# Kernel optimization log

Measured on AMD Instinct MI355X. Metric: run time of the kernel, lower is better.

Reference implementation:

```python
import jax, jax.numpy as jnp
import numpy as np
from functools import partial

IN_DIM = 128
NUM_HEADS = 8
DOWN_DIM = IN_DIM // 2          # 64
HEAD_DIM = DOWN_DIM // NUM_HEADS  # 8
MID = max(1, DOWN_DIM // 16)    # 4 (gate_reduce=16)
DIL = 3
BN_EPS = 1e-5


def conv2d(x, w, padding=0, dilation=1):
    # x: [B,C,H,W], w: [O,I,kh,kw]
    return jax.lax.conv_general_dilated(
        x, w, window_strides=(1, 1),
        padding=[(padding, padding), (padding, padding)],
        rhs_dilation=(dilation, dilation),
        dimension_numbers=("NCHW", "OIHW", "NCHW"))


def batchnorm(x, gamma, beta, mean, var):
    # inference-mode BN over channel dim
    scale = (gamma / jnp.sqrt(var + BN_EPS))[None, :, None, None]
    shift = (beta - mean * gamma / jnp.sqrt(var + BN_EPS))[None, :, None, None]
    return x * scale + shift


def complex_l2_norm(z, eps=1e-6):
    denom = jnp.sqrt(jnp.sum(z.real ** 2 + z.imag ** 2, axis=-1, keepdims=True) + eps)
    return z / denom


def complex_softmax(z):
    return jax.lax.complex(jax.nn.softmax(z.real, axis=-1),
                           jax.nn.softmax(z.imag, axis=-1))


def setup_inputs() -> dict:
    key = jax.random.key(0)
    ks = jax.random.split(key, 6)
    B, H, W = 8, 128, 128
    inp = {}
    inp["x"] = jax.random.normal(ks[0], (B, IN_DIM, H, W), dtype=jnp.float32)
    inp["conv_w"] = jax.random.normal(ks[1], (DOWN_DIM, IN_DIM, 3, 3), dtype=jnp.float32) * 0.02
    inp["bn1_g"] = jnp.ones((DOWN_DIM,), jnp.float32)
    inp["bn1_b"] = jnp.zeros((DOWN_DIM,), jnp.float32)
    inp["bn1_m"] = jnp.zeros((DOWN_DIM,), jnp.float32)
    inp["bn1_v"] = jnp.ones((DOWN_DIM,), jnp.float32)
    inp["cg1_w"] = jax.random.normal(ks[2], (MID, DOWN_DIM, 1, 1), dtype=jnp.float32) * 0.1
    inp["cg1_b"] = jnp.zeros((MID,), jnp.float32)
    inp["cgbn_g"] = jnp.ones((MID,), jnp.float32)
    inp["cgbn_b"] = jnp.zeros((MID,), jnp.float32)
    inp["cgbn_m"] = jnp.zeros((MID,), jnp.float32)
    inp["cgbn_v"] = jnp.ones((MID,), jnp.float32)
    inp["cg2_w"] = jax.random.normal(ks[3], (DOWN_DIM, MID, 1, 1), dtype=jnp.float32) * 0.1
    inp["cg2_b"] = jnp.zeros((DOWN_DIM,), jnp.float32)
    inp["tau"] = jnp.ones((NUM_HEADS, 1, 1), jnp.float32) * (HEAD_DIM ** -0.5)
    return inp


def reference(x, conv_w, bn1_g, bn1_b, bn1_m, bn1_v,
              cg1_w, cg1_b, cgbn_g, cgbn_b, cgbn_m, cgbn_v,
              cg2_w, cg2_b, tau):
    B, C, H, W = x.shape
    # reduce branch: dilated 3x3 conv -> BN -> GELU (exact, matching torch nn.GELU)
    feat = conv2d(x, conv_w, padding=DIL, dilation=DIL)
    feat = batchnorm(feat, bn1_g, bn1_b, bn1_m, bn1_v)
    feat = jax.nn.gelu(feat, approximate=False)

    # q=k=v=g = fft2(feat) (torch computes four identical FFTs; same math)
    F2 = jnp.fft.fft2(feat.astype(jnp.float32), axes=(-2, -1))  # complex64 [B,64,H,W]
    N = H * W
    qkv = F2.reshape(B, NUM_HEADS, HEAD_DIM, N)  # b h d (H W)
    q = complex_l2_norm(qkv)
    k = complex_l2_norm(qkv)
    v = qkv
    # attn: [b,h,d,d] — tiny; contraction over N
    attn = jnp.einsum("bhdn,bhen->bhde", q, jnp.conj(k)) * tau
    attn = complex_softmax(attn)
    out_f = jnp.einsum("bhde,bhen->bhdn", attn, v)
    out_f = out_f.reshape(B, DOWN_DIM, H, W)
    out_f = jnp.abs(jnp.fft.ifft2(out_f, axes=(-2, -1)))

    # gated branch on g = F2
    gr = F2.real
    cg = conv2d(gr, cg1_w) + cg1_b[None, :, None, None]
    cg = batchnorm(cg, cgbn_g, cgbn_b, cgbn_m, cgbn_v)
    cg = jax.nn.gelu(cg, approximate=False)
    cg = conv2d(cg, cg2_w) + cg2_b[None, :, None, None]
    cg = jax.nn.sigmoid(cg)
    gate = cg * F2  # real gate times complex spectrum
    gate = jnp.abs(jnp.fft.ifft2(gate, axes=(-2, -1)))

    y = jnp.concatenate([out_f, gate], axis=1)
    return y + x
```

## Files before the change

kernel.cpp:

```cpp
#include <hip/hip_runtime.h>
#include <hip/hip_bf16.h>
#include <math.h>

#define NB 8
#define CIN 128
#define CDN 64
#define NPIX 16384
#define NHEADS 8
#define HDIM 8

typedef __attribute__((ext_vector_type(8))) short bf16x8;
typedef __attribute__((ext_vector_type(4))) float f32x4;
typedef __attribute__((ext_vector_type(8))) unsigned short u16x8;

struct alignas(8) c2 { float x, y; };

__device__ inline c2 cadd(c2 a, c2 b){ return {a.x+b.x, a.y+b.y}; }
__device__ inline c2 csub(c2 a, c2 b){ return {a.x-b.x, a.y-b.y}; }
__device__ inline c2 cmul(c2 a, c2 b){ return {a.x*b.x - a.y*b.y, a.x*b.y + a.y*b.x}; }
__device__ inline c2 shfl2(c2 v, int m){ return { __shfl_xor(v.x, m, 64), __shfl_xor(v.y, m, 64) }; }
__device__ inline float gelu_exact(float v){ return 0.5f*v*(1.f + erff(v*0.70710678118654752f)); }
__device__ inline unsigned short f2bf(float f){
  __hip_bfloat16 h = __float2bfloat16(f);
  return *reinterpret_cast<unsigned short*>(&h);
}
__device__ inline float bf2f(unsigned short u){ return __uint_as_float((unsigned)u << 16); }

struct Tw { c2 t0; c2 t[6]; };
__device__ inline void tw_init(Tw& w, int t){
  float sn, cs;
  sincosf(-6.283185307179586f * (float)t * (1.f/128.f), &sn, &cs); w.t0 = {cs, sn};
  #pragma unroll
  for (int i = 0; i < 6; ++i) {
    int sp = 32 >> i;
    int j = t & (sp-1);
    sincosf(-3.141592653589793f * (float)j / (float)sp, &sn, &cs);
    w.t[i] = {cs, sn};
  }
}
__device__ inline void fft128_fwd(c2& a, c2& b, int t, const Tw& w){
  c2 s = cadd(a,b), d = csub(a,b);
  a = s; b = cmul(d, w.t0);
  #pragma unroll
  for (int i = 0; i < 6; ++i) {
    int sp = 32 >> i;
    c2 oa = shfl2(a, sp), ob = shfl2(b, sp);
    c2 tw = w.t[i];
    if (t & sp) { a = cmul(csub(oa,a), tw); b = cmul(csub(ob,b), tw); }
    else        { a = cadd(a,oa);           b = cadd(b,ob); }
  }
}
__device__ inline void fft128_inv(c2& a, c2& b, int t, const Tw& w){
  #pragma unroll
  for (int i = 5; i >= 0; --i) {
    int sp = 32 >> i;
    c2 tw = {w.t[i].x, -w.t[i].y};
    c2 oa = shfl2(a, sp), ob = shfl2(b, sp);
    if (t & sp) { a = csub(oa, cmul(a, tw)); b = csub(ob, cmul(b, tw)); }
    else        { a = cadd(a, cmul(oa, tw)); b = cadd(b, cmul(ob, tw)); }
  }
  c2 t0c = {w.t0.x, -w.t0.y};
  c2 wb = cmul(b, t0c);
  b = csub(a, wb);
  a = cadd(a, wb);
}

__device__ inline void gload_lds16(const void* g, void* l){
  __builtin_amdgcn_global_load_lds(
      (const __attribute__((address_space(1))) unsigned int*)g,
      (__attribute__((address_space(3))) unsigned int*)l, 16, 0, 0);
}

__device__ inline int colmap8(int wv, int i){
  if (wv == 0) return i;
  if (wv == 1) return 8 + i;
  if (wv == 2) return i < 4 ? 16 + i : 24 + i;
  if (wv == 3) return 20 + i;
  if (wv < 8) { int a = wv - 4; return i < 4 ? 32 + 4*a + i : 56 - 4*a + i; }
  int a = wv - 8; return i < 4 ? 64 + 4*a + i : 120 - 4*a + i;
}

__global__ __launch_bounds__(256) void k_wpack(const float* __restrict__ w, unsigned short* __restrict__ wP){
  int idx = blockIdx.x*256 + threadIdx.x;
  if (idx >= 4*9*64*32) return;
  int cc  = idx / 18432;
  int r   = idx - cc*18432;
  int tap = r / 2048;
  int r2  = r - tap*2048;
  int co  = r2 >> 5;
  int cil = r2 & 31;
  int ci  = cc*32 + cil;
  wP[idx] = f2bf(w[(co*CIN + ci)*9 + tap]);
}

__global__ __launch_bounds__(256) void k_xpose(const float* __restrict__ x, unsigned short* __restrict__ xT){
  int b = blockIdx.x >> 6;
  int px = (blockIdx.x & 63)*256 + threadIdx.x;
  const float* xb = x + (size_t)b*CIN*NPIX + px;
  #pragma unroll 2
  for (int ci0 = 0; ci0 < 128; ci0 += 8) {
    u16x8 v;
    #pragma unroll
    for (int j = 0; j < 8; ++j) v[j] = f2bf(xb[(size_t)(ci0+j)*NPIX]);
    int cc = ci0 >> 5;
    *(u16x8*)(xT + (((size_t)(b*4+cc)*NPIX + px)*32 + (ci0 & 31))) = v;
  }
}

__global__ __launch_bounds__(256) void k_conv(const unsigned short* __restrict__ xT,
    const unsigned short* __restrict__ wP,
    const float* __restrict__ bg, const float* __restrict__ bbeta,
    const float* __restrict__ bm, const float* __restrict__ bv,
    const float* __restrict__ w1,
    unsigned short* __restrict__ feat, float* __restrict__ u){
  __shared__ __align__(16) unsigned short sX[512*32];
  __shared__ float w1s[256];
  const int tid = threadIdx.x;
  const int bb   = blockIdx.z;
  const int half = blockIdx.x & 1;
  const int coBase = half*32;
  const int x0 = (blockIdx.x >> 1) * 16, y0 = blockIdx.y * 16;
  const int wv  = tid >> 6;
  const int l   = tid & 63;
  const int l15 = l & 15;
  const int g   = l >> 4;

  w1s[tid] = w1[tid];

  const bool interior = (x0 >= 16) && (x0 <= 96) && (y0 >= 16) && (y0 <= 96);

  f32x4 acc[2][4];
  #pragma unroll
  for (int m=0;m<2;++m)
    #pragma unroll
    for (int n=0;n<4;++n) acc[m][n] = {0.f,0.f,0.f,0.f};

  const int ko = g*8;

  for (int cc = 0; cc < 4; ++cc) {
    __syncthreads();
    const unsigned short* xcc = xT + ((size_t)(bb*4 + cc))*NPIX*32;
    if (interior) {
      #pragma unroll
      for (int k = 0; k < 8; ++k) {
        int blk = k*4 + wv;
        int idx = blk*64 + l;
        int p = idx >> 2, i = idx & 3;
        int pc = p < 484 ? p : 483;
        int py = pc / 22, px = pc - py*22;
        int gpix = (y0-3+py)*128 + (x0-3+px);
        int sg = i ^ ((p >> 1) & 3);
        const unsigned short* srcp = xcc + (size_t)gpix*32 + sg*8;
        gload_lds16(srcp, (char*)sX + blk*1024);
      }
    } else {
      #pragma unroll
      for (int k = 0; k < 8; ++k) {
        int idx = k*256 + tid;
        int p = idx >> 2, i = idx & 3;
        u16x8 v = {0,0,0,0,0,0,0,0};
        if (p < 484) {
          int py = p / 22, px = p - py*22;
          int gy = y0-3+py, gx = x0-3+px;
          if ((unsigned)gy < 128u && (unsigned)gx < 128u) {
            int sg = i ^ ((p >> 1) & 3);
            v = *(const u16x8*)(xcc + (size_t)(gy*128+gx)*32 + sg*8);
          }
        }
        *(u16x8*)((char*)sX + idx*16) = v;
      }
    }
    __syncthreads();

    const unsigned short* wcc = wP + cc*18432;
    for (int tap = 0; tap < 9; ++tap) {
      int dy = (tap/3)*3, dx = (tap - (tap/3)*3)*3;
      const unsigned short* wt = wcc + tap*2048;
      bf16x8 a[2], b[4];
      #pragma unroll
      for (int m = 0; m < 2; ++m)
        a[m] = *reinterpret_cast<const bf16x8*>(wt + (coBase + m*16 + l15)*32 + ko);
      #pragma unroll
      for (int n = 0; n < 4; ++n) {
        int p = (wv*4 + n + dy)*22 + l15 + dx;
        b[n] = *reinterpret_cast<const bf16x8*>(&sX[p*32 + ((g ^ ((p >> 1) & 3)) << 3)]);
      }
      #pragma unroll
      for (int m = 0; m < 2; ++m)
        #pragma unroll
        for (int n = 0; n < 4; ++n)
          acc[m][n] = __builtin_amdgcn_mfma_f32_16x16x32_bf16(a[m], b[n], acc[m][n], 0, 0, 0);
    }
  }

  float up[4][4];
  #pragma unroll
  for (int n=0;n<4;++n)
    #pragma unroll
    for (int m2=0;m2<4;++m2) up[n][m2] = 0.f;

  #pragma unroll
  for (int m = 0; m < 2; ++m) {
    #pragma unroll
    for (int r = 0; r < 4; ++r) {
      int co = coBase + m*16 + g*4 + r;
      float sc = bg[co] * rsqrtf(bv[co] + 1e-5f);
      float sh = bbeta[co] - bm[co]*sc;
      float wv4[4];
      #pragma unroll
      for (int m2 = 0; m2 < 4; ++m2) wv4[m2] = w1s[m2*64 + co];
      #pragma unroll
      for (int n = 0; n < 4; ++n) {
        int py = wv*4 + n;
        float v = gelu_exact(acc[m][n][r]*sc + sh);
        feat[((size_t)(bb*CDN + co)*128 + (y0+py))*128 + x0 + l15] = f2bf(v);
        #pragma unroll
        for (int m2 = 0; m2 < 4; ++m2) up[n][m2] += wv4[m2]*v;
      }
    }
  }
  #pragma unroll
  for (int n=0;n<4;++n)
    #pragma unroll
    for (int m2=0;m2<4;++m2) {
      up[n][m2] += __shfl_xor(up[n][m2], 16, 64);
      up[n][m2] += __shfl_xor(up[n][m2], 32, 64);
    }
  if (g == 0) {
    #pragma unroll
    for (int n = 0; n < 4; ++n) {
      int py = y0 + wv*4 + n;
      #pragma unroll
      for (int m2 = 0; m2 < 4; ++m2)
        u[((size_t)((bb*2 + half)*4 + m2))*NPIX + py*128 + x0 + l15] = up[n][m2];
    }
  }
}

__global__ __launch_bounds__(256) void k_attn1(const unsigned short* __restrict__ feat, float* __restrict__ part){
  int bh = blockIdx.x, ck = blockIdx.y;
  int b = bh >> 3, h = bh & 7;
  const unsigned short* f = feat + (size_t)(b*CDN + h*HDIM)*NPIX;
  float acc[36];
  #pragma unroll
  for (int i=0;i<36;++i) acc[i]=0.f;
  for (int p = ck*2048 + threadIdx.x; p < (ck+1)*2048; p += 256) {
    float v[8];
    #pragma unroll
    for (int d=0; d<8; ++d) v[d] = bf2f(f[d*NPIX + p]);
    int i = 0;
    #pragma unroll
    for (int d=0; d<8; ++d)
      #pragma unroll
      for (int e=0; e<=d; ++e) acc[i++] += v[d]*v[e];
  }
  #pragma unroll
  for (int i=0;i<36;++i)
    #pragma unroll
    for (int off=32; off; off>>=1) acc[i] += __shfl_xor(acc[i], off, 64);
  __shared__ float red[4][36];
  int wave = threadIdx.x >> 6, lane = threadIdx.x & 63;
  if (lane == 0) {
    #pragma unroll
    for (int i=0;i<36;++i) red[wave][i] = acc[i];
  }
  __syncthreads();
  if (threadIdx.x < 36)
    part[(bh*8+ck)*36 + threadIdx.x] =
      red[0][threadIdx.x]+red[1][threadIdx.x]+red[2][threadIdx.x]+red[3][threadIdx.x];
}

__global__ __launch_bounds__(64) void k_attn2(const float* __restrict__ part, const float* __restrict__ tau,
                                              float* __restrict__ attn){
  int bh = blockIdx.x; int h = bh & 7;
  __shared__ float Gm[36];
  int i = threadIdx.x;
  if (i < 36) {
    float s = 0.f;
    #pragma unroll
    for (int k = 0; k < 8; ++k) s += part[(bh*8+k)*36 + i];
    Gm[i] = s;
  }
  __syncthreads();
  if (i == 0) {
    float G[8][8];
    int c=0;
    for (int d=0;d<8;++d) for(int e=0;e<=d;++e){
      float s = Gm[c]; G[d][e]=s; G[e][d]=s; ++c;
    }
    float nrm[8];
    for (int d=0;d<8;++d) nrm[d] = sqrtf(16384.f*G[d][d] + 1e-6f);
    float tv = tau[h];
    for (int d=0;d<8;++d) {
      float row[8]; float mx = -1e30f;
      for (int e=0;e<8;++e){ row[e] = tv*16384.f*G[d][e]/(nrm[d]*nrm[e]); mx = fmaxf(mx,row[e]); }
      float s=0.f;
      for (int e=0;e<8;++e){ row[e] = expf(row[e]-mx); s += row[e]; }
      for (int e=0;e<8;++e) attn[bh*64 + d*8 + e] = row[e]/s;
    }
  }
}

__global__ __launch_bounds__(256) void k_outf(const unsigned short* __restrict__ feat, const float* __restrict__ attn,
                                              const float* __restrict__ x, float* __restrict__ out){
  int bh = blockIdx.x; int b = bh >> 3, h = bh & 7;
  int p = blockIdx.y*256 + threadIdx.x;
  __shared__ float A[64];
  if (threadIdx.x < 64) A[threadIdx.x] = attn[bh*64 + threadIdx.x];
  __syncthreads();
  const unsigned short* f = feat + (size_t)(b*CDN + h*HDIM)*NPIX;
  float v[8];
  #pragma unroll
  for (int e=0;e<8;++e) v[e] = bf2f(f[e*NPIX + p]);
  float im = 0.f;
  #pragma unroll
  for (int e=0;e<8;++e) im += v[e];
  im *= 0.125f;
  #pragma unroll
  for (int d=0;d<8;++d){
    float re = 0.f;
    #pragma unroll
    for (int e=0;e<8;++e) re += A[d*8+e]*v[e];
    size_t o = ((size_t)(b*CIN + h*HDIM + d))*NPIX + p;
    out[o] = sqrtf(re*re + im*im) + x[o];
  }
}

__global__ __launch_bounds__(512) void k_ufft(const float* __restrict__ u,
    const float* __restrict__ b1,
    const float* __restrict__ gg, const float* __restrict__ gbeta,
    const float* __restrict__ gm, const float* __restrict__ gv,
    float* __restrict__ mid){
  __shared__ c2 T[64*129];
  int b = blockIdx.x >> 2, m = blockIdx.x & 3;
  int tid = threadIdx.x, wv = tid >> 6, t = tid & 63;
  Tw w; tw_init(w, t);
  const float* src0 = u + (size_t)((b*2+0)*4+m)*NPIX;
  const float* src1 = u + (size_t)((b*2+1)*4+m)*NPIX;
  c2 ra[16], rb[16];
  #pragma unroll
  for (int i = 0; i < 16; ++i) {
    int y = wv*16 + i;
    ra[i] = {src0[y*128 + t] + src1[y*128 + t], 0.f};
    rb[i] = {src0[y*128 + t + 64] + src1[y*128 + t + 64], 0.f};
  }
  #pragma unroll
  for (int i = 0; i < 16; ++i) fft128_fwd(ra[i], rb[i], t, w);
  c2 ca[16], cb[16];
  if (wv < 4) {
    #pragma unroll
    for (int i = 0; i < 16; ++i) {
      int y = wv*16 + i;
      T[y*129 + t] = ra[i]; T[y*129 + t + 64] = rb[i];
    }
  }
  __syncthreads();
  #pragma unroll
  for (int i = 0; i < 16; ++i) ca[i] = T[t*129 + wv*16 + i];
  __syncthreads();
  if (wv >= 4) {
    #pragma unroll
    for (int i = 0; i < 16; ++i) {
      int y = (wv-4)*16 + i;
      T[y*129 + t] = ra[i]; T[y*129 + t + 64] = rb[i];
    }
  }
  __syncthreads();
  #pragma unroll
  for (int i = 0; i < 16; ++i) cb[i] = T[t*129 + wv*16 + i];
  #pragma unroll
  for (int i = 0; i < 16; ++i) fft128_fwd(ca[i], cb[i], t, w);
  float sc = gg[m]*rsqrtf(gv[m]+1e-5f);
  float sh = gbeta[m] - gm[m]*sc;
  float bb1 = b1[m];
  float* md = mid + (size_t)(b*4+m)*NPIX;
  #pragma unroll
  for (int i = 0; i < 16; ++i) {
    int kx = wv*16 + i;
    md[kx*128 + t]      = gelu_exact((ca[i].x + bb1)*sc + sh);
    md[kx*128 + t + 64] = gelu_exact((cb[i].x + bb1)*sc + sh);
  }
}

__global__ __launch_bounds__(256) void k_gmap(const float* __restrict__ mid, const float* __restrict__ w2,
                                              const float* __restrict__ b2, unsigned* __restrict__ gPack){
  __shared__ float w2s[256], b2s[64];
  w2s[threadIdx.x] = w2[threadIdx.x];
  if (threadIdx.x < 64) b2s[threadIdx.x] = b2[threadIdx.x];
  __syncthreads();
  int b = blockIdx.x >> 6;
  int k = (blockIdx.x & 63)*256 + threadIdx.x;
  const float* md = mid + (size_t)b*4*NPIX + k;
  float m0 = md[0], m1 = md[NPIX], m2 = md[2*NPIX], m3 = md[3*NPIX];
  unsigned* gp = gPack + (size_t)b*32*NPIX + k;
  #pragma unroll 8
  for (int cp = 0; cp < 32; ++cp) {
    float slo = b2s[cp]    + w2s[cp*4]*m0    + w2s[cp*4+1]*m1    + w2s[cp*4+2]*m2    + w2s[cp*4+3]*m3;
    float shi = b2s[cp+32] + w2s[(cp+32)*4]*m0 + w2s[(cp+32)*4+1]*m1 + w2s[(cp+32)*4+2]*m2 + w2s[(cp+32)*4+3]*m3;
    slo = 1.f/(1.f+expf(-slo));
    shi = 1.f/(1.f+expf(-shi));
    gp[(size_t)cp*NPIX] = ((unsigned)f2bf(shi) << 16) | (unsigned)f2bf(slo);
  }
}

__global__ __launch_bounds__(1024)
void k_fused(const unsigned short* __restrict__ feat, const unsigned* __restrict__ gPack,
             const float* __restrict__ x, float* __restrict__ out){
  __shared__ c2 T[128*129];
  int ib = blockIdx.x;
  int b = ib >> 5, c = ib & 31;
  int tid = threadIdx.x, wv = tid >> 6, t = tid & 63;
  Tw w; tw_init(w, t);
  int ta = __brev((64 - (__brev(t) >> 26)) & 63) >> 26;
  const unsigned short* srcA = feat + (size_t)(b*CDN + c)*NPIX;
  const unsigned short* srcB = feat + (size_t)(b*CDN + c + 32)*NPIX;
  const unsigned* gp = gPack + (size_t)(b*32 + c)*NPIX;

  c2 ra[8], rb[8];
  #pragma unroll
  for (int i = 0; i < 8; ++i) {
    int y = wv*8 + i;
    ra[i] = {bf2f(srcA[y*128 + t]),      bf2f(srcB[y*128 + t])};
    rb[i] = {bf2f(srcA[y*128 + t + 64]), bf2f(srcB[y*128 + t + 64])};
  }
  #pragma unroll
  for (int i = 0; i < 8; ++i) fft128_fwd(ra[i], rb[i], t, w);
  #pragma unroll
  for (int i = 0; i < 8; ++i) {
    int y = wv*8 + i;
    T[y*129 + t] = ra[i]; T[y*129 + t + 64] = rb[i];
  }
  __syncthreads();
  c2 ca[8], cb[8];
  #pragma unroll
  for (int i = 0; i < 8; ++i) {
    int s = colmap8(wv, i);
    ca[i] = T[t*129 + s];
    cb[i] = T[(t+64)*129 + s];
  }
  unsigned gwa[8], gwb[8];
  #pragma unroll
  for (int i = 0; i < 8; ++i) {
    int s = colmap8(wv, i);
    gwa[i] = gp[s*128 + t];
    gwb[i] = gp[s*128 + 64 + t];
  }
  #pragma unroll
  for (int i = 0; i < 8; ++i) fft128_fwd(ca[i], cb[i], t, w);

  #define GUN(w_, lo_, hi_) float lo_ = __uint_as_float((w_) << 16); float hi_ = __uint_as_float((w_) & 0xffff0000u);
  #define CPAIR(I, J) { \
    GUN(gwa[I], g1aI, g2aI); GUN(gwb[I], g1bI, g2bI); \
    GUN(gwa[J], g1aJ, g2aJ); GUN(gwb[J], g1bJ, g2bJ); \
    c2 paI = { __shfl(ca[J].x, ta, 64), -__shfl(ca[J].y, ta, 64) }; \
    c2 paJ = { __shfl(ca[I].x, ta, 64), -__shfl(ca[I].y, ta, 64) }; \
    c2 pbI = { __shfl_xor(cb[J].x, 63, 64), -__shfl_xor(cb[J].y, 63, 64) }; \
    c2 pbJ = { __shfl_xor(cb[I].x, 63, 64), -__shfl_xor(cb[I].y, 63, 64) }; \
    float gsaI=0.5f*(g1aI+g2aI), gdaI=0.5f*(g1aI-g2aI); \
    float gsaJ=0.5f*(g1aJ+g2aJ), gdaJ=0.5f*(g1aJ-g2aJ); \
    float gsbI=0.5f*(g1bI+g2bI), gdbI=0.5f*(g1bI-g2bI); \
    float gsbJ=0.5f*(g1bJ+g2bJ), gdbJ=0.5f*(g1bJ-g2bJ); \
    ca[I] = { gsaI*ca[I].x + gdaI*paI.x, gsaI*ca[I].y + gdaI*paI.y }; \
    ca[J] = { gsaJ*ca[J].x + gdaJ*paJ.x, gsaJ*ca[J].y + gdaJ*paJ.y }; \
    cb[I] = { gsbI*cb[I].x + gdbI*pbI.x, gsbI*cb[I].y + gdbI*pbI.y }; \
    cb[J] = { gsbJ*cb[J].x + gdbJ*pbJ.x, gsbJ*cb[J].y + gdbJ*pbJ.y }; \
  }
  #define CSELF(I) { \
    GUN(gwa[I], g1aI, g2aI); GUN(gwb[I], g1bI, g2bI); \
    c2 paI = { __shfl(ca[I].x, ta, 64), -__shfl(ca[I].y, ta, 64) }; \
    c2 pbI = { __shfl_xor(cb[I].x, 63, 64), -__shfl_xor(cb[I].y, 63, 64) }; \
    float gsaI=0.5f*(g1aI+g2aI), gdaI=0.5f*(g1aI-g2aI); \
    float gsbI=0.5f*(g1bI+g2bI), gdbI=0.5f*(g1bI-g2bI); \
    ca[I] = { gsaI*ca[I].x + gdaI*paI.x, gsaI*ca[I].y + gdaI*paI.y }; \
    cb[I] = { gsbI*cb[I].x + gdbI*pbI.x, gsbI*cb[I].y + gdbI*pbI.y }; \
  }
  if (wv == 0) {
    CSELF(0); CSELF(1);
    CPAIR(2,3); CPAIR(4,7); CPAIR(5,6);
  } else {
    CPAIR(0,7); CPAIR(1,6); CPAIR(2,5); CPAIR(3,4);
  }
  #undef CPAIR
  #undef CSELF
  #undef GUN

  #pragma unroll
  for (int i = 0; i < 8; ++i) fft128_inv(ca[i], cb[i], t, w);
  __syncthreads();
  #pragma unroll
  for (int i = 0; i < 8; ++i) {
    int s = colmap8(wv, i);
    T[t*129 + s] = ca[i];
    T[(t+64)*129 + s] = cb[i];
  }
  __syncthreads();
  #pragma unroll
  for (int i = 0; i < 8; ++i) {
    int y = wv*8 + i;
    ra[i] = T[y*129 + t];
    rb[i] = T[y*129 + t + 64];
  }
  #pragma unroll
  for (int i = 0; i < 8; ++i) fft128_inv(ra[i], rb[i], t, w);
  const float* xr1 = x + ((size_t)(b*CIN + 64 + c))*NPIX;
  const float* xr2 = x + ((size_t)(b*CIN + 96 + c))*NPIX;
  float* o1 = out + ((size_t)(b*CIN + 64 + c))*NPIX;
  float* o2 = out + ((size_t)(b*CIN + 96 + c))*NPIX;
  const float s = 1.f/16384.f;
  #pragma unroll
  for (int i = 0; i < 8; ++i) {
    int y = wv*8 + i;
    o1[y*128 + t]      = fabsf(ra[i].x)*s + xr1[y*128 + t];
    o1[y*128 + t + 64] = fabsf(rb[i].x)*s + xr1[y*128 + t + 64];
    o2[y*128 + t]      = fabsf(ra[i].y)*s + xr2[y*128 + t];
    o2[y*128 + t + 64] = fabsf(rb[i].y)*s + xr2[y*128 + t + 64];
  }
}

extern "C" void kernel_launch(void* const* d_in, const int* in_sizes, int n_in,
                              void* d_out, int out_size, void* d_ws, size_t ws_size,
                              hipStream_t stream){
  const float* x      = (const float*)d_in[0];
  const float* conv_w = (const float*)d_in[1];
  const float* bn1_g  = (const float*)d_in[2];
  const float* bn1_b  = (const float*)d_in[3];
  const float* bn1_m  = (const float*)d_in[4];
  const float* bn1_v  = (const float*)d_in[5];
  const float* cg1_w  = (const float*)d_in[6];
  const float* cg1_b  = (const float*)d_in[7];
  const float* cgbn_g = (const float*)d_in[8];
  const float* cgbn_b = (const float*)d_in[9];
  const float* cgbn_m = (const float*)d_in[10];
  const float* cgbn_v = (const float*)d_in[11];
  const float* cg2_w  = (const float*)d_in[12];
  const float* cg2_b  = (const float*)d_in[13];
  const float* tau    = (const float*)d_in[14];
  float* out = (float*)d_out;

  char* ws = (char*)d_ws;
  unsigned short* feat  = (unsigned short*)ws;
  unsigned short* xT    = (unsigned short*)(ws + 33554432);
  unsigned*       gPack = (unsigned*)(ws + 33554432);
  float*          u     = (float*)(ws + 67108864);
  float*          mid   = (float*)(ws + 71303168);
  unsigned short* wPack = (unsigned short*)(ws + 73400320);
  float*          attn  = (float*)(ws + 73547776);
  float*          part  = (float*)(ws + 73564160);

  k_wpack<<<288, 256, 0, stream>>>(conv_w, wPack);
  k_xpose<<<512, 256, 0, stream>>>(x, xT);
  k_conv<<<dim3(16,8,NB), 256, 0, stream>>>(xT, wPack, bn1_g, bn1_b, bn1_m, bn1_v, cg1_w, feat, u);
  k_ufft<<<NB*4, 512, 0, stream>>>(u, cg1_b, cgbn_g, cgbn_b, cgbn_m, cgbn_v, mid);
  k_gmap<<<NB*64, 256, 0, stream>>>(mid, cg2_w, cg2_b, gPack);
  k_attn1<<<dim3(NB*NHEADS, 8), 256, 0, stream>>>(feat, part);
  k_attn2<<<NB*NHEADS, 64, 0, stream>>>(part, tau, attn);
  k_outf<<<dim3(NB*NHEADS, 64), 256, 0, stream>>>(feat, attn, x, out);
  k_fused<<<NB*32, 1024, 0, stream>>>(feat, gPack, x, out);
}
```

Before: 206.1 us.

## Merge prep kernels, fold attention softmax into outf, remap conv block order

Merges the weight-pack and input-transpose kernels into one launch, and folds the small attention-softmax kernel into the output kernel so each block recomputes its head's 8x8 softmax from the partial Gram sums. It also remaps the conv block index so that blocks sharing the same spatial tile but different output-channel halves run adjacently, aiming for better L2 reuse of the input tile. This removes two launches and their serialization gaps. In exchange, every k_outf block (64 per head) redundantly runs a serial single-thread softmax.

Measured after the change: 210.9 us. +2.3%, slower.

```diff
diff --git a/kernel.cpp b/kernel.cpp
--- a/kernel.cpp
+++ b/kernel.cpp
@@ -80,30 +80,31 @@
   int a = wv - 8; return i < 4 ? 64 + 4*a + i : 120 - 4*a + i;
 }
 
-__global__ __launch_bounds__(256) void k_wpack(const float* __restrict__ w, unsigned short* __restrict__ wP){
-  int idx = blockIdx.x*256 + threadIdx.x;
-  if (idx >= 4*9*64*32) return;
-  int cc  = idx / 18432;
-  int r   = idx - cc*18432;
-  int tap = r / 2048;
-  int r2  = r - tap*2048;
-  int co  = r2 >> 5;
-  int cil = r2 & 31;
-  int ci  = cc*32 + cil;
-  wP[idx] = f2bf(w[(co*CIN + ci)*9 + tap]);
-}
-
-__global__ __launch_bounds__(256) void k_xpose(const float* __restrict__ x, unsigned short* __restrict__ xT){
-  int b = blockIdx.x >> 6;
-  int px = (blockIdx.x & 63)*256 + threadIdx.x;
-  const float* xb = x + (size_t)b*CIN*NPIX + px;
-  #pragma unroll 2
-  for (int ci0 = 0; ci0 < 128; ci0 += 8) {
-    u16x8 v;
-    #pragma unroll
-    for (int j = 0; j < 8; ++j) v[j] = f2bf(xb[(size_t)(ci0+j)*NPIX]);
-    int cc = ci0 >> 5;
-    *(u16x8*)(xT + (((size_t)(b*4+cc)*NPIX + px)*32 + (ci0 & 31))) = v;
+__global__ __launch_bounds__(256) void k_prep(const float* __restrict__ x, unsigned short* __restrict__ xT,
+                                              const float* __restrict__ w, unsigned short* __restrict__ wP){
+  if (blockIdx.x < 512) {
+    int b = blockIdx.x >> 6;
+    int px = (blockIdx.x & 63)*256 + threadIdx.x;
+    const float* xb = x + (size_t)b*CIN*NPIX + px;
+    #pragma unroll 2
+    for (int ci0 = 0; ci0 < 128; ci0 += 8) {
+      u16x8 v;
+      #pragma unroll
+      for (int j = 0; j < 8; ++j) v[j] = f2bf(xb[(size_t)(ci0+j)*NPIX]);
+      int cc = ci0 >> 5;
+      *(u16x8*)(xT + (((size_t)(b*4+cc)*NPIX + px)*32 + (ci0 & 31))) = v;
+    }
+  } else {
+    int idx = (blockIdx.x - 512)*256 + threadIdx.x;
+    if (idx >= 4*9*64*32) return;
+    int cc  = idx / 18432;
+    int r   = idx - cc*18432;
+    int tap = r / 2048;
+    int r2  = r - tap*2048;
+    int co  = r2 >> 5;
+    int cil = r2 & 31;
+    int ci  = cc*32 + cil;
+    wP[idx] = f2bf(w[(co*CIN + ci)*9 + tap]);
   }
 }
 
@@ -116,10 +117,13 @@
   __shared__ __align__(16) unsigned short sX[512*32];
   __shared__ float w1s[256];
   const int tid = threadIdx.x;
-  const int bb   = blockIdx.z;
-  const int half = blockIdx.x & 1;
+  const int flat = blockIdx.x + (blockIdx.y << 4) + (blockIdx.z << 7);
+  const int half = (flat >> 3) & 1;
+  const int tf   = (flat & 7) | ((flat >> 4) << 3);
+  const int x0 = (tf & 7) * 16;
+  const int y0 = ((tf >> 3) & 7) * 16;
+  const int bb = tf >> 6;
   const int coBase = half*32;
-  const int x0 = (blockIdx.x >> 1) * 16, y0 = blockIdx.y * 16;
   const int wv  = tid >> 6;
   const int l   = tid & 63;
   const int l15 = l & 15;
@@ -270,19 +274,21 @@
       red[0][threadIdx.x]+red[1][threadIdx.x]+red[2][threadIdx.x]+red[3][threadIdx.x];
 }
 
-__global__ __launch_bounds__(64) void k_attn2(const float* __restrict__ part, const float* __restrict__ tau,
-                                              float* __restrict__ attn){
-  int bh = blockIdx.x; int h = bh & 7;
+__global__ __launch_bounds__(256) void k_outf(const unsigned short* __restrict__ feat, const float* __restrict__ part,
+                                              const float* __restrict__ tau,
+                                              const float* __restrict__ x, float* __restrict__ out){
+  int bh = blockIdx.x; int b = bh >> 3, h = bh & 7;
+  int p = blockIdx.y*256 + threadIdx.x;
+  __shared__ float A[64];
   __shared__ float Gm[36];
-  int i = threadIdx.x;
-  if (i < 36) {
+  if (threadIdx.x < 36) {
     float s = 0.f;
     #pragma unroll
-    for (int k = 0; k < 8; ++k) s += part[(bh*8+k)*36 + i];
-    Gm[i] = s;
-  }
-  __syncthreads();
-  if (i == 0) {
+    for (int k = 0; k < 8; ++k) s += part[(bh*8+k)*36 + threadIdx.x];
+    Gm[threadIdx.x] = s;
+  }
+  __syncthreads();
+  if (threadIdx.x == 0) {
     float G[8][8];
     int c=0;
     for (int d=0;d<8;++d) for(int e=0;e<=d;++e){
@@ -296,17 +302,9 @@
       for (int e=0;e<8;++e){ row[e] = tv*16384.f*G[d][e]/(nrm[d]*nrm[e]); mx = fmaxf(mx,row[e]); }
       float s=0.f;
       for (int e=0;e<8;++e){ row[e] = expf(row[e]-mx); s += row[e]; }
-      for (int e=0;e<8;++e) attn[bh*64 + d*8 + e] = row[e]/s;
-    }
-  }
-}
-
-__global__ __launch_bounds__(256) void k_outf(const unsigned short* __restrict__ feat, const float* __restrict__ attn,
-                                              const float* __restrict__ x, float* __restrict__ out){
-  int bh = blockIdx.x; int b = bh >> 3, h = bh & 7;
-  int p = blockIdx.y*256 + threadIdx.x;
-  __shared__ float A[64];
-  if (threadIdx.x < 64) A[threadIdx.x] = attn[bh*64 + threadIdx.x];
+      for (int e=0;e<8;++e) A[d*8+e] = row[e]/s;
+    }
+  }
   __syncthreads();
   const unsigned short* f = feat + (size_t)(b*CDN + h*HDIM)*NPIX;
   float v[8];
@@ -544,16 +542,13 @@
   float*          u     = (float*)(ws + 67108864);
   float*          mid   = (float*)(ws + 71303168);
   unsigned short* wPack = (unsigned short*)(ws + 73400320);
-  float*          attn  = (float*)(ws + 73547776);
-  float*          part  = (float*)(ws + 73564160);
-
-  k_wpack<<<288, 256, 0, stream>>>(conv_w, wPack);
-  k_xpose<<<512, 256, 0, stream>>>(x, xT);
+  float*          part  = (float*)(ws + 73547776);
+
+  k_prep<<<800, 256, 0, stream>>>(x, xT, conv_w, wPack);
   k_conv<<<dim3(16,8,NB), 256, 0, stream>>>(xT, wPack, bn1_g, bn1_b, bn1_m, bn1_v, cg1_w, feat, u);
   k_ufft<<<NB*4, 512, 0, stream>>>(u, cg1_b, cgbn_g, cgbn_b, cgbn_m, cgbn_v, mid);
   k_gmap<<<NB*64, 256, 0, stream>>>(mid, cg2_w, cg2_b, gPack);
   k_attn1<<<dim3(NB*NHEADS, 8), 256, 0, stream>>>(feat, part);
-  k_attn2<<<NB*NHEADS, 64, 0, stream>>>(part, tau, attn);
-  k_outf<<<dim3(NB*NHEADS, 64), 256, 0, stream>>>(feat, attn, x, out);
+  k_outf<<<dim3(NB*NHEADS, 64), 256, 0, stream>>>(feat, part, tau, x, out);
   k_fused<<<NB*32, 1024, 0, stream>>>(feat, gPack, x, out);
 }
```
